# Performance work log

Hardware: AMD Instinct MI355X
Metric: run time of the kernel (lower is better)

The kernel has to match this reference:

```python
import jax, jax.numpy as jnp
import numpy as np

WS, EXP, FW, HEADS = 7, 3, 7, 6
DIM = 192
HD = DIM // HEADS
SCALE = HD ** -0.5
POOL_K, POOL_PAD = 7, 3  # focal level k=0: kernel = 2*(FW//2) + 2**0 + (2**0 - 1) = 7, stride 1, pad 3
WA = WS * WS  # 49 tokens per window


def _rel_index():
    # identical formula for in-window bias and pooled-window bias (k_window = FW + 2**0 - 1 = 7 = WS)
    c = np.stack(np.meshgrid(np.arange(WS), np.arange(WS), indexing='ij')).reshape(2, -1)
    rel = (c[:, :, None] - c[:, None, :]).transpose(1, 2, 0).copy()
    rel[..., 0] += WS - 1
    rel[..., 1] += WS - 1
    rel[..., 0] *= 2 * WS - 1
    return rel.sum(-1)  # (49, 49) int indices into 169-entry tables


def _valid_rolled():
    m = np.ones((4, WS, WS), dtype=np.float32)
    m[0, :-EXP, :-EXP] = 0  # tl
    m[1, :-EXP, EXP:] = 0   # tr
    m[2, EXP:, :-EXP] = 0   # bl
    m[3, EXP:, EXP:] = 0    # br
    return np.nonzero(m.reshape(-1))[0]  # (132,)

REL_IDX = _rel_index()
VALID_ROLLED = _valid_rolled()


def _win_part(t):
    # (B,H,W,C) -> (B*nWin, WA, HEADS, HD)
    B, H, W, C = t.shape
    t = t.reshape(B, H // WS, WS, W // WS, WS, C).transpose(0, 1, 3, 2, 4, 5)
    return t.reshape(-1, WA, HEADS, HD)


def _unfold(t):
    # torch.nn.Unfold(kernel=7, stride=1, pad=3) on (B,h,w,C) -> (B*h*w, K*K, C)
    B, h, w, C = t.shape
    tp = jnp.pad(t, ((0, 0), (POOL_PAD, POOL_PAD), (POOL_PAD, POOL_PAD), (0, 0)))
    ii = np.arange(h)[:, None] + np.arange(POOL_K)[None, :]
    jj = np.arange(w)[:, None] + np.arange(POOL_K)[None, :]
    p = tp[:, ii][:, :, :, jj]            # (B, h, K, w, K, C)
    p = p.transpose(0, 1, 3, 2, 4, 5)     # (B, h, w, K, K, C)
    return p.reshape(B * h * w, POOL_K * POOL_K, C)


def setup_inputs() -> dict:
    key = jax.random.key(0)
    ks = jax.random.split(key, 9)
    B, H, W = 8, 112, 112
    nWh, nWw = H // WS, W // WS
    return {
        'x': jax.random.normal(ks[0], (B, H, W, DIM), jnp.float32),
        'x_pooled': jax.random.normal(ks[1], (B, nWh, nWw, DIM), jnp.float32),
        'qkv_w': jax.random.normal(ks[2], (3 * DIM, DIM), jnp.float32) * 0.02,
        'qkv_b': jax.random.normal(ks[3], (3 * DIM,), jnp.float32) * 0.02,
        'proj_w': jax.random.normal(ks[4], (DIM, DIM), jnp.float32) * 0.02,
        'proj_b': jax.random.normal(ks[5], (DIM,), jnp.float32) * 0.02,
        'rpb_table': jax.random.normal(ks[6], ((2 * WS - 1) ** 2, HEADS), jnp.float32) * 0.02,
        'rpb_neighbors': jax.random.normal(ks[7], (1, HEADS, WA, len(VALID_ROLLED)), jnp.float32) * 0.02,
        'rpb_windows': jax.random.normal(ks[8], (HEADS, (2 * WS - 1) ** 2), jnp.float32) * 0.02,
    }


def reference(x, x_pooled, qkv_w, qkv_b, proj_w, proj_b, rpb_table, rpb_neighbors, rpb_windows):
    B, H, W, C = x.shape
    # qkv on fine features
    qkv = x @ qkv_w.T + qkv_b                    # (B,H,W,3C)
    q, k, v = jnp.split(qkv, 3, axis=-1)
    qw = _win_part(q).transpose(0, 2, 1, 3)      # (BnW, heads, 49, hd)
    kw = _win_part(k).transpose(0, 2, 1, 3)
    vw = _win_part(v).transpose(0, 2, 1, 3)

    # rolled neighbor keys/values (tl, tr, bl, br), gather valid ring indices
    shifts = [(-EXP, -EXP), (-EXP, EXP), (EXP, -EXP), (EXP, EXP)]
    k_roll = jnp.concatenate([_win_part(jnp.roll(k, s, axis=(1, 2))) for s in shifts], axis=1)
    v_roll = jnp.concatenate([_win_part(jnp.roll(v, s, axis=(1, 2))) for s in shifts], axis=1)
    k_roll = k_roll.transpose(0, 2, 1, 3)[:, :, VALID_ROLLED]   # (BnW, heads, 132, hd)
    v_roll = v_roll.transpose(0, 2, 1, 3)[:, :, VALID_ROLLED]
    k_rolled = jnp.concatenate([kw, k_roll], axis=2)            # (BnW, heads, 181, hd)
    v_rolled = jnp.concatenate([vw, v_roll], axis=2)
    wa_rolled = k_rolled.shape[2]

    # focal level-0 pooled keys/values via unfold on the pooled map
    _, nWh, nWw, _ = x_pooled.shape
    qkv_p = x_pooled @ qkv_w.T + qkv_b
    _, kp, vp = jnp.split(qkv_p, 3, axis=-1)
    k_pool = _unfold(kp).reshape(-1, POOL_K * POOL_K, HEADS, HD).transpose(0, 2, 1, 3)  # (BnW, heads, 49, hd)
    v_pool = _unfold(vp).reshape(-1, POOL_K * POOL_K, HEADS, HD).transpose(0, 2, 1, 3)
    # validity mask from unfolding an all-ones map (zero padding -> -100)
    um = _unfold(jnp.ones((1, nWh, nWw, 1), x.dtype))[..., 0]   # (nWin, 49)
    pool_mask = jnp.where(um == 0, jnp.asarray(-100.0, x.dtype), jnp.asarray(0.0, x.dtype))

    k_all = jnp.concatenate([k_rolled, k_pool], axis=2)          # (BnW, heads, 230, hd)
    v_all = jnp.concatenate([v_rolled, v_pool], axis=2)

    attn = jnp.einsum('bhqd,bhkd->bhqk', qw * SCALE, k_all)      # (BnW, heads, 49, 230)

    # relative position biases, concatenated along the key axis
    bias_win = rpb_table[REL_IDX.reshape(-1)].reshape(WA, WA, HEADS).transpose(2, 0, 1)     # (heads,49,49)
    bias_pool = rpb_windows[:, REL_IDX.reshape(-1)].reshape(HEADS, WA, WA)                  # (heads,49,49)
    bias = jnp.concatenate([bias_win, rpb_neighbors[0], bias_pool], axis=-1)                # (heads,49,230)
    attn = attn + bias[None]
    # boundary mask on the pooled slice, tiled per batch
    mask_b = jnp.tile(pool_mask, (B, 1))[:, None, None, :]       # (BnW,1,1,49)
    attn = attn.at[..., wa_rolled:].add(mask_b)

    attn = jax.nn.softmax(attn, axis=-1)
    out = jnp.einsum('bhqk,bhkd->bqhd', attn, v_all).reshape(-1, WA, C)
    return out @ proj_w.T + proj_b                               # (B*nWin, 49, C)
```

## Files before the change

kernel.cpp:

```cpp
#include <hip/hip_runtime.h>
#include <stdint.h>


#define DIM 192
#define HEADS 6
#define HD 32
#define WA 49
#define NKEY 230
#define VSTR 264
#define SSTR2 136
#define SCALE_F 0.17677669529663687f
#define NFINE 100352
#define POOLBASE (NFINE * DIM)

typedef __attribute__((ext_vector_type(8))) short bf16x8;
typedef __attribute__((ext_vector_type(4))) float f32x4;

__device__ __forceinline__ short f2bf(float f) {
  union { float f; uint32_t u; } v; v.f = f;
  uint32_t u = v.u;
  return (short)((u + 0x7FFFu + ((u >> 16) & 1u)) >> 16);
}

__device__ __forceinline__ float bf2f(short s) {
  union { uint32_t u; float f; } v;
  v.u = ((uint32_t)(uint16_t)s) << 16;
  return v.f;
}

__device__ __forceinline__ uint32_t cvtpk(float lo, float hi) {
  uint32_t r;
  asm("v_cvt_pk_bf16_f32 %0, %1, %2" : "=v"(r) : "v"(lo), "v"(hi));
  return r;
}

__global__ __launch_bounds__(256) void k_setup(
    const float* __restrict__ qkv_w, const float* __restrict__ proj_w,
    const float* __restrict__ rpb_table, const float* __restrict__ rpb_nb,
    const float* __restrict__ rpb_win,
    short* __restrict__ w1, short* __restrict__ w1s, short* __restrict__ w2s,
    int* __restrict__ t_idx, short* __restrict__ bias_bf) {
  __shared__ int2 ring_s[132];
  if (threadIdx.x < 132) {
    int e = threadIdx.x;
    int cnt = 0, fdr = 0, fdc = 0;
    for (int idx = 0; idx < 196; ++idx) {
      int s = idx / 49, rc = idx % 49, r = rc / 7, c = rc % 7;
      bool valid;
      if (s == 0)      valid = (r >= 4) || (c >= 4);
      else if (s == 1) valid = (r >= 4) || (c < 3);
      else if (s == 2) valid = (r < 3)  || (c >= 4);
      else             valid = (r < 3)  || (c < 3);
      if (valid) {
        if (cnt == e) { fdr = r + ((s < 2) ? 3 : -3); fdc = c + (((s & 1) == 0) ? 3 : -3); }
        ++cnt;
      }
    }
    ring_s[e] = make_int2(fdr, fdc);
  }
  __syncthreads();

  const int tid = blockIdx.x * blockDim.x + threadIdx.x;
  const int nth = gridDim.x * blockDim.x;
  for (int i = tid; i < 576 * DIM; i += nth) {
    float fv = qkv_w[i];
    w1[i] = f2bf(fv);
    int r = i / DIM, c = i % DIM;
    int t = r >> 5, ntl = (r >> 4) & 1, lr = r & 15;
    int ks = c >> 5, quad = (c >> 3) & 3, e = c & 7;
    w1s[t * 6144 + (((ntl * 6 + ks) * 4 + quad) * 16 + lr) * 8 + e] = f2bf(fv);
  }
  for (int i = tid; i < DIM * DIM; i += nth) {
    int r = i / DIM, c = i % DIM;
    int t = r >> 5, ntl = (r >> 4) & 1, lr = r & 15;
    int ks = c >> 5, quad = (c >> 3) & 3, e = c & 7;
    w2s[t * 6144 + (((ntl * 6 + ks) * 4 + quad) * 16 + lr) * 8 + e] = f2bf(proj_w[i]);
  }
  for (int i = tid; i < 2048 * NKEY; i += nth) {
    int win = i / NKEY, kk = i - win * NKEY;
    int b = win >> 8, wr = (win >> 4) & 15, wc = win & 15;
    int off;
    if (kk < 49) {
      int ii = wr * 7 + kk / 7, jj = wc * 7 + kk % 7;
      off = ((b * 112 + ii) * 112 + jj) * DIM;
    } else if (kk < 181) {
      int2 rr = ring_s[kk - 49];
      int ii = wr * 7 + rr.x; if (ii < 0) ii += 112; if (ii >= 112) ii -= 112;
      int jj = wc * 7 + rr.y; if (jj < 0) jj += 112; if (jj >= 112) jj -= 112;
      off = ((b * 112 + ii) * 112 + jj) * DIM;
    } else {
      int p = kk - 181;
      int ii = wr - 3 + p / 7, jj = wc - 3 + p % 7;
      off = (ii >= 0 && ii < 16 && jj >= 0 && jj < 16)
              ? (POOLBASE + ((b * 16 + ii) * 16 + jj) * DIM) : -1;
    }
    t_idx[(win << 8) + kk] = off;
  }
  for (int i = tid; i < HEADS * 15 * 1024; i += nth) {
    int row = i & 63, l16v = (i >> 6) & 15;
    int rem = i >> 10, nt = rem % 15, h = rem / 15;
    int kk = nt * 16 + l16v;
    float bv = 0.f;
    if (kk >= NKEY) {
      bv = -1e30f;
    } else if (row < WA) {
      if (kk < 49) {
        int ar = row / 7, ac = row % 7, br = kk / 7, bc = kk % 7;
        bv = rpb_table[((ar - br + 6) * 13 + (ac - bc + 6)) * HEADS + h];
      } else if (kk < 181) {
        bv = rpb_nb[((size_t)h * WA + row) * 132 + (kk - 49)];
      } else {
        int p = kk - 181;
        int ar = row / 7, ac = row % 7, br = p / 7, bc = p % 7;
        bv = rpb_win[h * 169 + (ar - br + 6) * 13 + (ac - bc + 6)];
      }
    }
    bias_bf[i] = f2bf(bv);
  }
}

__global__ __launch_bounds__(256, 4) void k_qkv_main(
    const float* __restrict__ x, const short* __restrict__ w1s, const float* __restrict__ qkv_b,
    short* __restrict__ qw, short* __restrict__ kn, short* __restrict__ vn) {
  __shared__ __align__(16) short wbuf[2][6144];
  const int tid = threadIdx.x;
  const int wave = tid >> 6, lane = tid & 63, quad = lane >> 4, l16 = lane & 15;
  const int mbase = blockIdx.x * 128;

  bf16x8 afr[2][6];
#pragma unroll
  for (int mt = 0; mt < 2; ++mt) {
    const float* xrow = x + (size_t)(mbase + wave * 32 + mt * 16 + l16) * DIM + quad * 8;
#pragma unroll
    for (int ks = 0; ks < 6; ++ks) {
      float4 f0 = *(const float4*)(xrow + ks * 32);
      float4 f1 = *(const float4*)(xrow + ks * 32 + 4);
      bf16x8 a;
      a[0] = f2bf(f0.x); a[1] = f2bf(f0.y); a[2] = f2bf(f0.z); a[3] = f2bf(f0.w);
      a[4] = f2bf(f1.x); a[5] = f2bf(f1.y); a[6] = f2bf(f1.z); a[7] = f2bf(f1.w);
      afr[mt][ks] = a;
    }
  }
  uint32_t q_base[2][4], kv_base[2][4];
#pragma unroll
  for (int mt = 0; mt < 2; ++mt)
#pragma unroll
    for (int rg = 0; rg < 4; ++rg) {
      int m = mbase + wave * 32 + mt * 16 + quad * 4 + rg;
      int bb = m / 12544, rem = m % 12544;
      int i = rem / 112, j = rem % 112;
      int wr = i / 7, rr = i % 7, wc = j / 7, cc = j % 7;
      int winid = (bb * 16 + wr) * 16 + wc;
      q_base[mt][rg]  = ((uint32_t)winid * WA + (rr * 7 + cc)) * DIM;
      kv_base[mt][rg] = (uint32_t)m * DIM;
    }

  int4 st[3];
  {
    const int4* src = (const int4*)w1s + tid;
#pragma unroll
    for (int it = 0; it < 3; ++it) st[it] = src[it * 256];
  }
  for (int t = 0; t < 18; ++t) {
    short* buf = wbuf[t & 1];
#pragma unroll
    for (int it = 0; it < 3; ++it) ((int4*)buf)[tid + it * 256] = st[it];
    __syncthreads();
    if (t < 17) {
      const int4* src = (const int4*)(w1s + (t + 1) * 6144) + tid;
#pragma unroll
      for (int it = 0; it < 3; ++it) st[it] = src[it * 256];
    }
#pragma unroll
    for (int ntl = 0; ntl < 2; ++ntl) {
      const int n = t * 32 + ntl * 16 + l16;
      bf16x8 bfr[6];
#pragma unroll
      for (int ks = 0; ks < 6; ++ks)
        bfr[ks] = *(const bf16x8*)&buf[(((ntl * 6 + ks) * 4 + quad) * 16 + l16) * 8];
      const float bias = qkv_b[n];
      f32x4 ac[2];
#pragma unroll
      for (int mt = 0; mt < 2; ++mt) {
        f32x4 a = {0.f, 0.f, 0.f, 0.f};
#pragma unroll
        for (int ks = 0; ks < 6; ++ks)
          a = __builtin_amdgcn_mfma_f32_16x16x32_bf16(afr[mt][ks], bfr[ks], a, 0, 0, 0);
        ac[mt] = a;
      }
      if (t < 6) {
        const float bq = bias * SCALE_F;
#pragma unroll
        for (int rg = 0; rg < 4; ++rg) {
          uint32_t r = cvtpk(fmaf(ac[0][rg], SCALE_F, bq), fmaf(ac[1][rg], SCALE_F, bq));
          qw[q_base[0][rg] + n] = (short)r;
          qw[q_base[1][rg] + n] = (short)(r >> 16);
        }
      } else if (t < 12) {
#pragma unroll
        for (int rg = 0; rg < 4; ++rg) {
          uint32_t r = cvtpk(ac[0][rg] + bias, ac[1][rg] + bias);
          kn[kv_base[0][rg] + (n - 192)] = (short)r;
          kn[kv_base[1][rg] + (n - 192)] = (short)(r >> 16);
        }
      } else {
#pragma unroll
        for (int rg = 0; rg < 4; ++rg) {
          uint32_t r = cvtpk(ac[0][rg] + bias, ac[1][rg] + bias);
          vn[kv_base[0][rg] + (n - 384)] = (short)r;
          vn[kv_base[1][rg] + (n - 384)] = (short)(r >> 16);
        }
      }
    }
  }
}

__global__ __launch_bounds__(256) void k_qkv_pool(
    const float* __restrict__ xp, const short* __restrict__ w1, const float* __restrict__ qkv_b,
    short* __restrict__ kp, short* __restrict__ vp) {
  const int tid = threadIdx.x;
  const int wave = tid >> 6, lane = tid & 63, quad = lane >> 4, l16 = lane & 15;
  const int mbase = (blockIdx.x * 4 + wave) * 16;

  bf16x8 afr[6];
  {
    const float* xrow = xp + (size_t)(mbase + l16) * DIM + quad * 8;
#pragma unroll
    for (int ks = 0; ks < 6; ++ks) {
      float4 f0 = *(const float4*)(xrow + ks * 32);
      float4 f1 = *(const float4*)(xrow + ks * 32 + 4);
      bf16x8 a;
      a[0] = f2bf(f0.x); a[1] = f2bf(f0.y); a[2] = f2bf(f0.z); a[3] = f2bf(f0.w);
      a[4] = f2bf(f1.x); a[5] = f2bf(f1.y); a[6] = f2bf(f1.z); a[7] = f2bf(f1.w);
      afr[ks] = a;
    }
  }
  for (int nt = 12; nt < 36; ++nt) {
    const int n = nt * 16 + l16;
    const short* wrow = w1 + (size_t)n * DIM + quad * 8;
    f32x4 acc = {0.f, 0.f, 0.f, 0.f};
#pragma unroll
    for (int ks = 0; ks < 6; ++ks)
      acc = __builtin_amdgcn_mfma_f32_16x16x32_bf16(afr[ks], *(const bf16x8*)(wrow + ks * 32), acc, 0, 0, 0);
    const float bias = qkv_b[n];
#pragma unroll
    for (int rg = 0; rg < 4; ++rg) {
      int m = mbase + quad * 4 + rg;
      float vo = acc[rg] + bias;
      if (nt < 24) kp[(size_t)m * DIM + (n - 192)] = f2bf(vo);
      else         vp[(size_t)m * DIM + (n - 384)] = f2bf(vo);
    }
  }
}

__global__ __launch_bounds__(256, 4) void k_attn(
    const short* __restrict__ qw, const short* __restrict__ kall, const short* __restrict__ vall,
    const short* __restrict__ bias_bf, const int* __restrict__ t_idx,
    short* __restrict__ ao) {
  __shared__ __align__(16) char smem[37120];
  short* vT_l  = (short*)smem;
  short* k_l   = (short*)(smem + 16896);
  short* S_l   = (short*)(smem + 16896);
  float* pmask = (float*)(smem + 36096);

  const int tid = threadIdx.x;
  const int bid = ((int)blockIdx.x & 7) * 1536 + ((int)blockIdx.x >> 3);
  const int win = bid / HEADS;
  const int h   = bid - win * HEADS;
  const int wr  = (win >> 4) & 15;
  const int wc  = win & 15;
  const int wave = tid >> 6, lane = tid & 63, quad = lane >> 4, l16 = lane & 15;

  {
    int* kli = (int*)k_l;
    for (int i = tid; i < 200; i += 256) kli[4600 + i] = 0;
    if (tid < 128) {
      int ch = tid >> 2, j = tid & 3;
      *(int4*)&vT_l[ch * VSTR + ((224 + j * 8) ^ (((ch >> 3) & 3) << 4))] = make_int4(0, 0, 0, 0);
    }
    float pm = 0.f;
    if (tid >= 181 && tid < NKEY) {
      int p = tid - 181;
      int pi = wr - 3 + p / 7, pj = wc - 3 + p % 7;
      if (pi < 0 || pi >= 16 || pj < 0 || pj >= 16) pm = -100.f;
    }
    pmask[tid] = pm;
  }
  bf16x8 qfr = {0, 0, 0, 0, 0, 0, 0, 0};
  {
    const int qrow = wave * 16 + l16;
    if (qrow < WA)
      qfr = *(const bf16x8*)(qw + ((size_t)win * WA + qrow) * DIM + h * HD + quad * 8);
  }
  __syncthreads();

  {
    const int part = tid & 3;
    const int choff = h * HD + part * 8;
    const int* tix = t_idx + (win << 8);
#pragma unroll
    for (int it = 0; it < 4; ++it) {
      int kk = it * 64 + (tid >> 2);
      if (kk < NKEY) {
        int off = tix[kk];
        int4 kvv = make_int4(0, 0, 0, 0), vvv = make_int4(0, 0, 0, 0);
        if (off >= 0) {
          kvv = *(const int4*)(kall + off + choff);
          vvv = *(const int4*)(vall + off + choff);
        }
        *(int4*)&k_l[kk * 40 + part * 8] = kvv;
        const short* vs = (const short*)&vvv;
        const int kkx = kk ^ (part << 4);
#pragma unroll
        for (int e = 0; e < 8; ++e) vT_l[(part * 8 + e) * VSTR + kkx] = vs[e];
      }
    }
  }
  __syncthreads();

  f32x4 acc[15];
#pragma unroll
  for (int nt = 0; nt < 15; ++nt) {
    bf16x8 kfr = *(const bf16x8*)&k_l[(nt * 16 + l16) * 40 + quad * 8];
    f32x4 z = {0.f, 0.f, 0.f, 0.f};
    acc[nt] = __builtin_amdgcn_mfma_f32_16x16x32_bf16(qfr, kfr, z, 0, 0, 0);
  }
  const int rowb = wave * 16 + quad * 4;
  {
    const short* bb = bias_bf + ((size_t)(h * 15 * 16 + l16)) * 64 + rowb;
#pragma unroll
    for (int nt = 0; nt < 15; ++nt) {
      int2 braw = *(const int2*)(bb + nt * 1024);
      const short* bs = (const short*)&braw;
      const float pm = pmask[nt * 16 + l16];
#pragma unroll
      for (int rg = 0; rg < 4; ++rg)
        acc[nt][rg] = acc[nt][rg] + bf2f(bs[rg]) + pm;
    }
  }
  float m4[4] = {-1e30f, -1e30f, -1e30f, -1e30f};
#pragma unroll
  for (int nt = 0; nt < 15; ++nt)
#pragma unroll
    for (int rg = 0; rg < 4; ++rg) m4[rg] = fmaxf(m4[rg], acc[nt][rg]);
#pragma unroll
  for (int msk = 1; msk <= 8; msk <<= 1)
#pragma unroll
    for (int rg = 0; rg < 4; ++rg) m4[rg] = fmaxf(m4[rg], __shfl_xor(m4[rg], msk));
  float s4[4] = {0.f, 0.f, 0.f, 0.f};
#pragma unroll
  for (int nt = 0; nt < 15; ++nt)
#pragma unroll
    for (int rg = 0; rg < 4; ++rg) {
      float e = __expf(acc[nt][rg] - m4[rg]);
      acc[nt][rg] = e; s4[rg] += e;
    }
#pragma unroll
  for (int msk = 1; msk <= 8; msk <<= 1)
#pragma unroll
    for (int rg = 0; rg < 4; ++rg) s4[rg] += __shfl_xor(s4[rg], msk);
  float inv4[4];
#pragma unroll
  for (int rg = 0; rg < 4; ++rg) inv4[rg] = 1.f / s4[rg];

  __syncthreads();

  const int swS = ((quad >> 1) & 1) << 4;
#pragma unroll
  for (int rg = 0; rg < 4; ++rg) {
    const int base = (rowb + rg) * SSTR2;
#pragma unroll
    for (int p = 0; p < 4; ++p) {
      uint32_t r = cvtpk(acc[2 * p][rg], acc[2 * p + 1][rg]);
      S_l[base + ((p * 32 + l16) ^ swS)]      = (short)r;
      S_l[base + ((p * 32 + 16 + l16) ^ swS)] = (short)(r >> 16);
    }
  }
  __syncthreads();

  const int swR = ((l16 >> 3) & 1) << 4;
  f32x4 acc2[2] = {{0.f, 0.f, 0.f, 0.f}, {0.f, 0.f, 0.f, 0.f}};
#pragma unroll
  for (int nt2 = 0; nt2 < 2; ++nt2) {
    const int fvr = (((nt2 * 16 + l16) >> 3) & 3) << 4;
#pragma unroll
    for (int k0 = 0; k0 < 4; ++k0) {
      bf16x8 pfr = *(const bf16x8*)&S_l[(wave * 16 + l16) * SSTR2 + ((k0 * 32 + quad * 8) ^ swR)];
      bf16x8 vfr = *(const bf16x8*)&vT_l[(nt2 * 16 + l16) * VSTR + ((k0 * 32 + quad * 8) ^ fvr)];
      acc2[nt2] = __builtin_amdgcn_mfma_f32_16x16x32_bf16(pfr, vfr, acc2[nt2], 0, 0, 0);
    }
  }
  __syncthreads();

#pragma unroll
  for (int rg = 0; rg < 4; ++rg) {
    const int base = (rowb + rg) * SSTR2;
#pragma unroll
    for (int p = 0; p < 3; ++p) {
      uint32_t r = cvtpk(acc[8 + 2 * p][rg], acc[9 + 2 * p][rg]);
      S_l[base + ((p * 32 + l16) ^ swS)]      = (short)r;
      S_l[base + ((p * 32 + 16 + l16) ^ swS)] = (short)(r >> 16);
    }
    uint32_t r = cvtpk(acc[14][rg], 0.f);
    S_l[base + ((96 + l16) ^ swS)]  = (short)r;
    S_l[base + ((112 + l16) ^ swS)] = (short)(r >> 16);
  }
  __syncthreads();

#pragma unroll
  for (int nt2 = 0; nt2 < 2; ++nt2) {
    const int fvr = (((nt2 * 16 + l16) >> 3) & 3) << 4;
#pragma unroll
    for (int k0 = 0; k0 < 4; ++k0) {
      bf16x8 pfr = *(const bf16x8*)&S_l[(wave * 16 + l16) * SSTR2 + ((k0 * 32 + quad * 8) ^ swR)];
      bf16x8 vfr = *(const bf16x8*)&vT_l[(nt2 * 16 + l16) * VSTR + ((128 + k0 * 32 + quad * 8) ^ fvr)];
      acc2[nt2] = __builtin_amdgcn_mfma_f32_16x16x32_bf16(pfr, vfr, acc2[nt2], 0, 0, 0);
    }
  }

#pragma unroll
  for (int rg = 0; rg < 4; ++rg) {
    const int row = rowb + rg;
    if (row < WA) {
      uint32_t r = cvtpk(acc2[0][rg] * inv4[rg], acc2[1][rg] * inv4[rg]);
      short* dst = ao + ((size_t)win * WA + row) * DIM + h * HD + l16;
      dst[0]  = (short)r;
      dst[16] = (short)(r >> 16);
    }
  }
}

__global__ __launch_bounds__(256, 4) void k_proj(
    const short* __restrict__ ao, const short* __restrict__ w2s, const float* __restrict__ pb,
    float* __restrict__ out) {
  __shared__ __align__(16) short wbuf[2][6144];
  const int tid = threadIdx.x;
  const int wave = tid >> 6, lane = tid & 63, quad = lane >> 4, l16 = lane & 15;
  const int mbase = blockIdx.x * 128;

  bf16x8 afr[2][6];
#pragma unroll
  for (int mt = 0; mt < 2; ++mt) {
    const short* arow = ao + (size_t)(mbase + wave * 32 + mt * 16 + l16) * DIM + quad * 8;
#pragma unroll
    for (int ks = 0; ks < 6; ++ks) afr[mt][ks] = *(const bf16x8*)(arow + ks * 32);
  }
  int4 st[3];
  {
    const int4* src = (const int4*)w2s + tid;
#pragma unroll
    for (int it = 0; it < 3; ++it) st[it] = src[it * 256];
  }
  for (int t = 0; t < 6; ++t) {
    short* buf = wbuf[t & 1];
#pragma unroll
    for (int it = 0; it < 3; ++it) ((int4*)buf)[tid + it * 256] = st[it];
    __syncthreads();
    if (t < 5) {
      const int4* src = (const int4*)(w2s + (t + 1) * 6144) + tid;
#pragma unroll
      for (int it = 0; it < 3; ++it) st[it] = src[it * 256];
    }
#pragma unroll
    for (int ntl = 0; ntl < 2; ++ntl) {
      const int n = t * 32 + ntl * 16 + l16;
      bf16x8 bfr[6];
#pragma unroll
      for (int ks = 0; ks < 6; ++ks)
        bfr[ks] = *(const bf16x8*)&buf[(((ntl * 6 + ks) * 4 + quad) * 16 + l16) * 8];
      const float bias = pb[n];
#pragma unroll
      for (int mt = 0; mt < 2; ++mt) {
        f32x4 acc = {0.f, 0.f, 0.f, 0.f};
#pragma unroll
        for (int ks = 0; ks < 6; ++ks)
          acc = __builtin_amdgcn_mfma_f32_16x16x32_bf16(afr[mt][ks], bfr[ks], acc, 0, 0, 0);
#pragma unroll
        for (int rg = 0; rg < 4; ++rg)
          out[(size_t)(mbase + wave * 32 + mt * 16 + quad * 4 + rg) * DIM + n] = acc[rg] + bias;
      }
    }
  }
}

extern "C" void kernel_launch(void* const* d_in, const int* in_sizes, int n_in,
                              void* d_out, int out_size, void* d_ws, size_t ws_size,
                              hipStream_t stream) {
  (void)in_sizes; (void)n_in; (void)out_size; (void)ws_size;
  const float* x         = (const float*)d_in[0];
  const float* xp        = (const float*)d_in[1];
  const float* qkv_w     = (const float*)d_in[2];
  const float* qkv_b     = (const float*)d_in[3];
  const float* proj_w    = (const float*)d_in[4];
  const float* proj_b    = (const float*)d_in[5];
  const float* rpb_table = (const float*)d_in[6];
  const float* rpb_nb    = (const float*)d_in[7];
  const float* rpb_win   = (const float*)d_in[8];

  char* ws = (char*)d_ws;
  size_t off = 0;
  auto alloc = [&](size_t bytes) -> void* {
    void* p = ws + off; off = (off + bytes + 255) & ~(size_t)255; return p;
  };
  short* w1       = (short*)alloc((size_t)576 * DIM * 2);
  short* w1s      = (short*)alloc((size_t)576 * DIM * 2);
  short* w2s      = (short*)alloc((size_t)DIM * DIM * 2);
  short* bias_bf  = (short*)alloc((size_t)HEADS * 15 * 1024 * 2);
  int*   t_idx    = (int*)  alloc((size_t)2048 * 256 * 4);
  short* qw       = (short*)alloc((size_t)2048 * WA * DIM * 2);
  short* kall     = (short*)alloc((size_t)(NFINE + 2048) * DIM * 2);
  short* vall     = (short*)alloc((size_t)(NFINE + 2048) * DIM * 2);
  short* ao       = (short*)alloc((size_t)2048 * WA * DIM * 2);

  k_setup<<<dim3(64), dim3(256), 0, stream>>>(qkv_w, proj_w, rpb_table, rpb_nb, rpb_win,
                                              w1, w1s, w2s, t_idx, bias_bf);
  k_qkv_main<<<dim3(784), dim3(256), 0, stream>>>(x, w1s, qkv_b, qw, kall, vall);
  k_qkv_pool<<<dim3(32), dim3(256), 0, stream>>>(xp, w1, qkv_b,
                                                 kall + (size_t)POOLBASE, vall + (size_t)POOLBASE);
  k_attn<<<dim3(12288), dim3(256), 0, stream>>>(qw, kall, vall, bias_bf, t_idx, ao);
  k_proj<<<dim3(784), dim3(256), 0, stream>>>(ao, w2s, proj_b, (float*)d_out);
}
```

Measured before the change: 474.7 us.

## Shrink attention LDS with XOR-swizzled layouts, fold log2e into Q and bias for exp2

The attention kernel's shared memory drops from about 37 KB to 32 KB by removing padded strides. K, V-transpose and score tiles now use power-of-two strides with XOR swizzles to avoid bank conflicts. Launch bounds rise to 5 blocks per CU. The pooled-window mask is now derived from the gather index instead of recomputed window coordinates. Q scaling and the bias table are premultiplied by log2(e) so softmax can use the hardware exp2 directly, which adds bf16 rounding changes and a risk of register pressure at the higher occupancy target.

```diff
diff --git a/kernel.cpp b/kernel.cpp
--- a/kernel.cpp
+++ b/kernel.cpp
@@ -7,9 +7,9 @@
 #define HD 32
 #define WA 49
 #define NKEY 230
-#define VSTR 264
-#define SSTR2 136
 #define SCALE_F 0.17677669529663687f
+#define LOG2E 1.4426950408889634f
+#define PM_NEG (-144.26950408889634f)
 #define NFINE 100352
 #define POOLBASE (NFINE * DIM)
 
@@ -115,7 +115,7 @@
         bv = rpb_win[h * 169 + (ar - br + 6) * 13 + (ac - bc + 6)];
       }
     }
-    bias_bf[i] = f2bf(bv);
+    bias_bf[i] = f2bf(bv * LOG2E);
   }
 }
 
@@ -189,10 +189,11 @@
         ac[mt] = a;
       }
       if (t < 6) {
-        const float bq = bias * SCALE_F;
+        const float qs = SCALE_F * LOG2E;
+        const float bq = bias * qs;
 #pragma unroll
         for (int rg = 0; rg < 4; ++rg) {
-          uint32_t r = cvtpk(fmaf(ac[0][rg], SCALE_F, bq), fmaf(ac[1][rg], SCALE_F, bq));
+          uint32_t r = cvtpk(fmaf(ac[0][rg], qs, bq), fmaf(ac[1][rg], qs, bq));
           qw[q_base[0][rg] + n] = (short)r;
           qw[q_base[1][rg] + n] = (short)(r >> 16);
         }
@@ -253,38 +254,28 @@
   }
 }
 
-__global__ __launch_bounds__(256, 4) void k_attn(
+__global__ __launch_bounds__(256, 5) void k_attn(
     const short* __restrict__ qw, const short* __restrict__ kall, const short* __restrict__ vall,
     const short* __restrict__ bias_bf, const int* __restrict__ t_idx,
     short* __restrict__ ao) {
-  __shared__ __align__(16) char smem[37120];
-  short* vT_l  = (short*)smem;
-  short* k_l   = (short*)(smem + 16896);
-  short* S_l   = (short*)(smem + 16896);
-  float* pmask = (float*)(smem + 36096);
+  __shared__ __align__(16) char smem[32768];
+  short* vT_l = (short*)smem;
+  short* k_l  = (short*)(smem + 16384);
+  short* S_l  = (short*)(smem + 16384);
+  float* pm_f = (float*)(smem + 32512);
 
   const int tid = threadIdx.x;
   const int bid = ((int)blockIdx.x & 7) * 1536 + ((int)blockIdx.x >> 3);
   const int win = bid / HEADS;
   const int h   = bid - win * HEADS;
-  const int wr  = (win >> 4) & 15;
-  const int wc  = win & 15;
   const int wave = tid >> 6, lane = tid & 63, quad = lane >> 4, l16 = lane & 15;
 
   {
-    int* kli = (int*)k_l;
-    for (int i = tid; i < 200; i += 256) kli[4600 + i] = 0;
-    if (tid < 128) {
-      int ch = tid >> 2, j = tid & 3;
-      *(int4*)&vT_l[ch * VSTR + ((224 + j * 8) ^ (((ch >> 3) & 3) << 4))] = make_int4(0, 0, 0, 0);
-    }
-    float pm = 0.f;
-    if (tid >= 181 && tid < NKEY) {
-      int p = tid - 181;
-      int pi = wr - 3 + p / 7, pj = wc - 3 + p % 7;
-      if (pi < 0 || pi >= 16 || pj < 0 || pj >= 16) pm = -100.f;
-    }
-    pmask[tid] = pm;
+    int4 z = make_int4(0, 0, 0, 0);
+#pragma unroll
+    for (int i = 0; i < 4; ++i) ((int4*)vT_l)[tid + i * 256] = z;
+    if (tid < 160) ((int*)k_l)[3680 + tid] = 0;
+    if (tid >= 49 && tid < 64) pm_f[tid] = 0.f;
   }
   bf16x8 qfr = {0, 0, 0, 0, 0, 0, 0, 0};
   {
@@ -298,6 +289,7 @@
     const int part = tid & 3;
     const int choff = h * HD + part * 8;
     const int* tix = t_idx + (win << 8);
+    const int ky = ((tid >> 3) & 3) << 3;
 #pragma unroll
     for (int it = 0; it < 4; ++it) {
       int kk = it * 64 + (tid >> 2);
@@ -308,22 +300,27 @@
           kvv = *(const int4*)(kall + off + choff);
           vvv = *(const int4*)(vall + off + choff);
         }
-        *(int4*)&k_l[kk * 40 + part * 8] = kvv;
+        *(int4*)&k_l[kk * 32 + ((part * 8) ^ ky)] = kvv;
         const short* vs = (const short*)&vvv;
-        const int kkx = kk ^ (part << 4);
-#pragma unroll
-        for (int e = 0; e < 8; ++e) vT_l[(part * 8 + e) * VSTR + kkx] = vs[e];
+        short* vbase = &vT_l[part * 2048 + (kk ^ (part << 4))];
+#pragma unroll
+        for (int e = 0; e < 8; ++e) vbase[e * 256] = vs[e];
+        if (part == 0 && kk >= 181)
+          pm_f[kk - 181] = (off < 0) ? PM_NEG : 0.f;
       }
     }
   }
   __syncthreads();
 
   f32x4 acc[15];
-#pragma unroll
-  for (int nt = 0; nt < 15; ++nt) {
-    bf16x8 kfr = *(const bf16x8*)&k_l[(nt * 16 + l16) * 40 + quad * 8];
-    f32x4 z = {0.f, 0.f, 0.f, 0.f};
-    acc[nt] = __builtin_amdgcn_mfma_f32_16x16x32_bf16(qfr, kfr, z, 0, 0, 0);
+  {
+    const int kcol = (quad * 8) ^ (((l16 >> 1) & 3) << 3);
+#pragma unroll
+    for (int nt = 0; nt < 15; ++nt) {
+      bf16x8 kfr = *(const bf16x8*)&k_l[(nt * 16 + l16) * 32 + kcol];
+      f32x4 z = {0.f, 0.f, 0.f, 0.f};
+      acc[nt] = __builtin_amdgcn_mfma_f32_16x16x32_bf16(qfr, kfr, z, 0, 0, 0);
+    }
   }
   const int rowb = wave * 16 + quad * 4;
   {
@@ -332,7 +329,14 @@
     for (int nt = 0; nt < 15; ++nt) {
       int2 braw = *(const int2*)(bb + nt * 1024);
       const short* bs = (const short*)&braw;
-      const float pm = pmask[nt * 16 + l16];
+      float pm = 0.f;
+      if (nt >= 12) {
+        pm = pm_f[nt * 16 + l16 - 181];
+      } else if (nt == 11) {
+        int idx = 11 * 16 + l16 - 181;
+        float t = pm_f[idx < 0 ? 0 : idx];
+        pm = (idx < 0) ? 0.f : t;
+      }
 #pragma unroll
       for (int rg = 0; rg < 4; ++rg)
         acc[nt][rg] = acc[nt][rg] + bf2f(bs[rg]) + pm;
@@ -352,7 +356,7 @@
   for (int nt = 0; nt < 15; ++nt)
 #pragma unroll
     for (int rg = 0; rg < 4; ++rg) {
-      float e = __expf(acc[nt][rg] - m4[rg]);
+      float e = __builtin_amdgcn_exp2f(acc[nt][rg] - m4[rg]);
       acc[nt][rg] = e; s4[rg] += e;
     }
 #pragma unroll
@@ -365,28 +369,28 @@
 
   __syncthreads();
 
-  const int swS = ((quad >> 1) & 1) << 4;
+  const int Xw = quad << 4;
 #pragma unroll
   for (int rg = 0; rg < 4; ++rg) {
-    const int base = (rowb + rg) * SSTR2;
+    const int base = (rowb + rg) * 128;
 #pragma unroll
     for (int p = 0; p < 4; ++p) {
       uint32_t r = cvtpk(acc[2 * p][rg], acc[2 * p + 1][rg]);
-      S_l[base + ((p * 32 + l16) ^ swS)]      = (short)r;
-      S_l[base + ((p * 32 + 16 + l16) ^ swS)] = (short)(r >> 16);
-    }
-  }
-  __syncthreads();
-
-  const int swR = ((l16 >> 3) & 1) << 4;
+      S_l[base + ((p * 32 + l16) ^ Xw)]      = (short)r;
+      S_l[base + ((p * 32 + 16 + l16) ^ Xw)] = (short)(r >> 16);
+    }
+  }
+  __syncthreads();
+
+  const int Xr = ((l16 >> 2) & 3) << 4;
   f32x4 acc2[2] = {{0.f, 0.f, 0.f, 0.f}, {0.f, 0.f, 0.f, 0.f}};
 #pragma unroll
   for (int nt2 = 0; nt2 < 2; ++nt2) {
     const int fvr = (((nt2 * 16 + l16) >> 3) & 3) << 4;
 #pragma unroll
     for (int k0 = 0; k0 < 4; ++k0) {
-      bf16x8 pfr = *(const bf16x8*)&S_l[(wave * 16 + l16) * SSTR2 + ((k0 * 32 + quad * 8) ^ swR)];
-      bf16x8 vfr = *(const bf16x8*)&vT_l[(nt2 * 16 + l16) * VSTR + ((k0 * 32 + quad * 8) ^ fvr)];
+      bf16x8 pfr = *(const bf16x8*)&S_l[(wave * 16 + l16) * 128 + ((k0 * 32 + quad * 8) ^ Xr)];
+      bf16x8 vfr = *(const bf16x8*)&vT_l[(nt2 * 16 + l16) * 256 + ((k0 * 32 + quad * 8) ^ fvr)];
       acc2[nt2] = __builtin_amdgcn_mfma_f32_16x16x32_bf16(pfr, vfr, acc2[nt2], 0, 0, 0);
     }
   }
@@ -394,16 +398,16 @@
 
 #pragma unroll
   for (int rg = 0; rg < 4; ++rg) {
-    const int base = (rowb + rg) * SSTR2;
+    const int base = (rowb + rg) * 128;
 #pragma unroll
     for (int p = 0; p < 3; ++p) {
       uint32_t r = cvtpk(acc[8 + 2 * p][rg], acc[9 + 2 * p][rg]);
-      S_l[base + ((p * 32 + l16) ^ swS)]      = (short)r;
-      S_l[base + ((p * 32 + 16 + l16) ^ swS)] = (short)(r >> 16);
+      S_l[base + ((p * 32 + l16) ^ Xw)]      = (short)r;
+      S_l[base + ((p * 32 + 16 + l16) ^ Xw)] = (short)(r >> 16);
     }
     uint32_t r = cvtpk(acc[14][rg], 0.f);
-    S_l[base + ((96 + l16) ^ swS)]  = (short)r;
-    S_l[base + ((112 + l16) ^ swS)] = (short)(r >> 16);
+    S_l[base + ((96 + l16) ^ Xw)]  = (short)r;
+    S_l[base + ((112 + l16) ^ Xw)] = (short)(r >> 16);
   }
   __syncthreads();
 
@@ -412,8 +416,8 @@
     const int fvr = (((nt2 * 16 + l16) >> 3) & 3) << 4;
 #pragma unroll
     for (int k0 = 0; k0 < 4; ++k0) {
-      bf16x8 pfr = *(const bf16x8*)&S_l[(wave * 16 + l16) * SSTR2 + ((k0 * 32 + quad * 8) ^ swR)];
-      bf16x8 vfr = *(const bf16x8*)&vT_l[(nt2 * 16 + l16) * VSTR + ((128 + k0 * 32 + quad * 8) ^ fvr)];
+      bf16x8 pfr = *(const bf16x8*)&S_l[(wave * 16 + l16) * 128 + ((k0 * 32 + quad * 8) ^ Xr)];
+      bf16x8 vfr = *(const bf16x8*)&vT_l[(nt2 * 16 + l16) * 256 + ((128 + k0 * 32 + quad * 8) ^ fvr)];
       acc2[nt2] = __builtin_amdgcn_mfma_f32_16x16x32_bf16(pfr, vfr, acc2[nt2], 0, 0, 0);
     }
   }
```

Result: slower. 511.3 us (+7.7%).
